# Optimization experiments

Measured on AMD Instinct MI355X. Metric: run time of the kernel, lower is better.

## Reference

```python
import jax, jax.numpy as jnp
import numpy as np

MARGIN = 1.0
EPS = 1e-6
DIAG_BIG = 99999.0


def setup_inputs() -> dict:
    key = jax.random.key(0)
    x = jax.random.normal(key, (16384, 256), dtype=jnp.float32)
    # HardNet descriptors are unit-L2 normalized (the distance formula assumes it)
    x = x / jnp.linalg.norm(x, axis=1, keepdims=True)
    return {"x": x}


def reference(x) -> jnp.ndarray:
    cnt = x.shape[0] // 2
    a = x[:cnt]          # [N, d] anchors
    p = x[cnt:]          # [N, d] positives
    # pairwise unit-L2 distance: sqrt((1 - a.p^T + eps) * 2)
    dmat = jnp.sqrt((1.0 - jnp.matmul(a, p.T) + EPS) * 2.0)  # [N, N]
    pos = jnp.diagonal(dmat)                                  # [N]
    # mask diagonal with large constant, then row/col mins = hard negatives
    masked = dmat + jnp.eye(cnt, dtype=dmat.dtype) * DIAG_BIG
    min_a = jnp.min(masked, axis=0)   # best negative anchor per positive
    min_p = jnp.min(masked, axis=1)   # best negative positive per anchor
    neg = jnp.minimum(min_a, min_p)   # [N]
    return jnp.mean(jnp.clip(MARGIN - neg + pos, 0.0))
```

## Files before the change

kernel.cpp:

```cpp
#include <hip/hip_runtime.h>
#include <hip/hip_fp8.h>


#define CNT    8192
#define KDIM   256
#define BIGF   3.0e38f
#define SCALE1 0x7F7F7F7F

typedef float f32x4  __attribute__((ext_vector_type(4)));
typedef float f32x16 __attribute__((ext_vector_type(16)));
typedef int   v8i    __attribute__((ext_vector_type(8)));

union frag8 { uint4 q[2]; v8i v; };

__device__ __forceinline__ unsigned short f2bf(float f) {
    unsigned u = __float_as_uint(f);
    u += 0x7FFFu + ((u >> 16) & 1u);
    return (unsigned short)(u >> 16);
}

__device__ __forceinline__ unsigned cvt4_fp8(float a, float b, float c, float d) {
#if __has_builtin(__builtin_amdgcn_cvt_pk_fp8_f32)
    unsigned v = __builtin_amdgcn_cvt_pk_fp8_f32(a, b, 0, false);
    v = __builtin_amdgcn_cvt_pk_fp8_f32(c, d, v, true);
    return v;
#else
    return (unsigned)__hip_fp8_e4m3(a).__x |
           ((unsigned)__hip_fp8_e4m3(b).__x << 8) |
           ((unsigned)__hip_fp8_e4m3(c).__x << 16) |
           ((unsigned)__hip_fp8_e4m3(d).__x << 24);
#endif
}


__global__ __launch_bounds__(256) void convert_mx_kernel(
    const float* __restrict__ x, unsigned char* __restrict__ xb,
    unsigned* __restrict__ mins)
{
    int T    = blockIdx.x * 256 + threadIdx.x;
    int lane = T & 63;
    int h    = (T >> 6) & 1;
    int c    = T >> 7;
    int kc64 = c & 3;
    int rg   = c >> 2;
    int row  = rg * 32 + (lane & 31);
    int col0 = kc64 * 64 + (lane >> 5) * 32 + h * 16;
    const float* src = x + (size_t)row * KDIM + col0;
    float4 u0 = *(const float4*)(src);
    float4 u1 = *(const float4*)(src + 4);
    float4 u2 = *(const float4*)(src + 8);
    float4 u3 = *(const float4*)(src + 12);
    uint4 w;
    w.x = cvt4_fp8(u0.x, u0.y, u0.z, u0.w);
    w.y = cvt4_fp8(u1.x, u1.y, u1.z, u1.w);
    w.z = cvt4_fp8(u2.x, u2.y, u2.z, u2.w);
    w.w = cvt4_fp8(u3.x, u3.y, u3.z, u3.w);
    *(uint4*)(xb + (size_t)T * 16) = w;
    if (T < 2 * CNT) mins[T] = 0x7F7FFFFFu;
}

__device__ __forceinline__ void stage_P(
    const char* __restrict__ Pb, char* lbuf, int bn, int wave, int lane)
{
    #pragma unroll
    for (int t = 0; t < 16; t++) {
        const int o   = wave * 16 + t;
        const int cc  = o >> 1;
        const int h   = o & 1;
        const int rg  = cc & 7;
        const int kcs = cc >> 3;
        const char* src = Pb + (((size_t)(bn * 8 + rg)) << 13)
                             + kcs * 2048 + h * 1024 + lane * 16;
        __builtin_amdgcn_global_load_lds(
            (const __attribute__((address_space(1))) void*)src,
            (__attribute__((address_space(3))) void*)(lbuf + cc * 2048 + h * 1024),
            16, 0, 0);
    }
}

#define TST  136
__global__ __launch_bounds__(256, 2) void dist12_kernel(
    const unsigned char* __restrict__ Ab_, const unsigned char* __restrict__ Pb_,
    unsigned* __restrict__ g_rowmin, unsigned* __restrict__ g_colmin,
    float* __restrict__ g_pos)
{
    __shared__ char smem[65536];

    const char* Ab = (const char*)Ab_;
    const char* Pb = (const char*)Pb_;

    const int tid  = threadIdx.x;
    const int l    = blockIdx.x;
    const int xcd  = l & 7;
    const int i    = l >> 3;
    const int bm   = (xcd >> 1) * 16 + (i & 15);
    const int bn   = (xcd & 1) * 16 + (i >> 4);

    const int wave = tid >> 6;
    const int lane = tid & 63;
    const int l31  = lane & 31;
    const int kh   = lane >> 5;
    const int wm   = wave >> 1;
    const int wn   = wave & 1;

    stage_P(Pb, smem, bn, wave, lane);
    __syncthreads();

    f32x16 acc[2][4];
    #pragma unroll
    for (int a = 0; a < 2; a++)
        #pragma unroll
        for (int b = 0; b < 4; b++)
            #pragma unroll
            for (int r = 0; r < 16; r++)
                acc[a][b][r] = 0.f;

    const char* Abase = Ab + lane * 16;
    size_t a_off[2];
    #pragma unroll
    for (int mi = 0; mi < 2; mi++)
        a_off[mi] = (size_t)(bm * 4 + wm * 2 + mi) << 13;

    frag8 ca[2], na[2];
    #pragma unroll
    for (int mi = 0; mi < 2; mi++) {
        ca[mi].q[0] = *(const uint4*)(Abase + a_off[mi]);
        ca[mi].q[1] = *(const uint4*)(Abase + a_off[mi] + 1024);
    }
    #pragma unroll
    for (int kc = 0; kc < 4; kc++) {
        if (kc < 3) {
            #pragma unroll
            for (int mi = 0; mi < 2; mi++) {
                na[mi].q[0] = *(const uint4*)(Abase + a_off[mi] + (kc + 1) * 2048);
                na[mi].q[1] = *(const uint4*)(Abase + a_off[mi] + (kc + 1) * 2048 + 1024);
            }
        }
        frag8 fb[4];
        #pragma unroll
        for (int ni = 0; ni < 4; ni++) {
            const char* p = smem + (kc * 8 + wn * 4 + ni) * 2048 + lane * 16;
            fb[ni].q[0] = *(const uint4*)(p);
            fb[ni].q[1] = *(const uint4*)(p + 1024);
        }
        #pragma unroll
        for (int mi = 0; mi < 2; mi++)
            #pragma unroll
            for (int ni = 0; ni < 4; ni++)
                acc[mi][ni] = __builtin_amdgcn_mfma_scale_f32_32x32x64_f8f6f4(
                    ca[mi].v, fb[ni].v, acc[mi][ni],
                    0, 0,
                    0, SCALE1,
                    0, SCALE1);
        if (kc < 3) {
            #pragma unroll
            for (int mi = 0; mi < 2; mi++) ca[mi] = na[mi];
        }
    }


    if ((bm >> 1) == bn) {
        const int dstart = (bm & 1) * 128;
        #pragma unroll
        for (int mi = 0; mi < 2; mi++)
            #pragma unroll
            for (int ni = 0; ni < 4; ni++)
                #pragma unroll
                for (int reg = 0; reg < 16; reg++) {
                    int rl = wm * 64 + mi * 32 + (reg & 3) + 8 * (reg >> 2) + 4 * kh;
                    int cl = wn * 128 + ni * 32 + l31;
                    if (cl == rl + dstart) {
                        g_pos[bm * 128 + rl] = (1.0f - acc[mi][ni][reg] + 1e-6f) * 2.0f;
                        acc[mi][ni][reg] = -BIGF;
                    }
                }
    }

    #pragma unroll
    for (int ni = 0; ni < 4; ni++) {
        float v = -BIGF;
        #pragma unroll
        for (int mi = 0; mi < 2; mi++)
            #pragma unroll
            for (int reg = 0; reg < 16; reg++)
                v = fmaxf(v, acc[mi][ni][reg]);
        v = fmaxf(v, __shfl_xor(v, 32, 64));
        if (kh == 0) {
            float tt = fmaxf((1.0f - v + 1e-6f) * 2.0f, 0.0f);
            atomicMin(&g_colmin[bn * 256 + wn * 128 + ni * 32 + l31],
                      __float_as_uint(tt));
        }
    }

    __syncthreads();
    float* T = (float*)smem;
    const int entry = wn * 32 + l31;
    #pragma unroll
    for (int mi = 0; mi < 2; mi++)
        #pragma unroll
        for (int q = 0; q < 4; q++) {
            f32x4 v;
            #pragma unroll
            for (int rr = 0; rr < 4; rr++) {
                float m = acc[mi][0][q * 4 + rr];
                #pragma unroll
                for (int ni = 1; ni < 4; ni++)
                    m = fmaxf(m, acc[mi][ni][q * 4 + rr]);
                v[rr] = m;
            }
            *(f32x4*)&T[entry * TST + wm * 64 + mi * 32 + q * 8 + kh * 4] = v;
        }
    __syncthreads();

    if (tid < 128) {
        int row = tid;
        float v0 = T[row], v1 = T[TST + row];
        #pragma unroll
        for (int e = 2; e < 64; e += 2) {
            v0 = fmaxf(v0, T[e * TST + row]);
            v1 = fmaxf(v1, T[(e + 1) * TST + row]);
        }
        float v = fmaxf(v0, v1);
        float tt = fmaxf((1.0f - v + 1e-6f) * 2.0f, 0.0f);
        atomicMin(&g_rowmin[bm * 128 + row], __float_as_uint(tt));
    }
}

__global__ __launch_bounds__(1024) void finalize_t_kernel(
    const unsigned* __restrict__ rm, const unsigned* __restrict__ cm,
    const float* __restrict__ post, float* __restrict__ out)
{
    float local = 0.f;
    for (int i = threadIdx.x; i < CNT; i += 1024) {
        float t   = fminf(__uint_as_float(rm[i]), __uint_as_float(cm[i]));
        float neg = sqrtf(fmaxf(t, 0.f));
        float pos = sqrtf(fmaxf(post[i], 0.f));
        local += fmaxf(1.0f - neg + pos, 0.0f);
    }
    #pragma unroll
    for (int m = 1; m < 64; m <<= 1) local += __shfl_xor(local, m, 64);
    __shared__ float wsum[16];
    if ((threadIdx.x & 63) == 0) wsum[threadIdx.x >> 6] = local;
    __syncthreads();
    if (threadIdx.x == 0) {
        float s = 0.f;
        #pragma unroll
        for (int w = 0; w < 16; w++) s += wsum[w];
        out[0] = s * (1.0f / (float)CNT);
    }
}


#define BM 128
#define BN 128
#define BK 64
#define KST (BK + 8)

typedef __bf16 bf16x8 __attribute__((ext_vector_type(8)));

__global__ __launch_bounds__(256) void init_min_kernel(unsigned* buf, int n) {
    int i = blockIdx.x * 256 + threadIdx.x;
    if (i < n) buf[i] = 0x7F7FFFFFu;
}

__global__ __launch_bounds__(256) void dist_tile_kernel(
    const float* __restrict__ A, const float* __restrict__ P,
    unsigned* __restrict__ g_rowmin, unsigned* __restrict__ g_colmin,
    float* __restrict__ g_pos)
{
    __shared__ unsigned short As[BM * KST];
    __shared__ unsigned short Bs[BN * KST];
    __shared__ unsigned redrow[BM];
    __shared__ unsigned redcol[BN];

    const int tid  = threadIdx.x;
    const int bm   = blockIdx.y;
    const int bn   = blockIdx.x;
    const int wave = tid >> 6;
    const int lane = tid & 63;
    const int quad = lane >> 4;
    const int l15  = lane & 15;
    const int m_off = (wave >> 1) * 64;
    const int n_off = (wave & 1) * 64;

    if (tid < BM) redrow[tid] = 0x7F7FFFFFu;
    if (tid < BN) redcol[tid] = 0x7F7FFFFFu;

    f32x4 acc[4][4];
    #pragma unroll
    for (int i = 0; i < 4; i++)
        #pragma unroll
        for (int j = 0; j < 4; j++)
            acc[i][j] = (f32x4){0.f, 0.f, 0.f, 0.f};

    const int srow = tid >> 4;
    const int scol = tid & 15;

    for (int kc = 0; kc < KDIM / BK; kc++) {
        #pragma unroll
        for (int i = 0; i < 8; i++) {
            int r = srow + i * 16;
            float4 va = *(const float4*)(A + (size_t)(bm * BM + r) * KDIM + kc * BK + scol * 4);
            float4 vb = *(const float4*)(P + (size_t)(bn * BN + r) * KDIM + kc * BK + scol * 4);
            ushort4 wa, wb;
            wa.x = f2bf(va.x); wa.y = f2bf(va.y); wa.z = f2bf(va.z); wa.w = f2bf(va.w);
            wb.x = f2bf(vb.x); wb.y = f2bf(vb.y); wb.z = f2bf(vb.z); wb.w = f2bf(vb.w);
            *(ushort4*)(&As[r * KST + scol * 4]) = wa;
            *(ushort4*)(&Bs[r * KST + scol * 4]) = wb;
        }
        __syncthreads();
        #pragma unroll
        for (int ks = 0; ks < BK / 32; ks++) {
            bf16x8 af[4], bfr[4];
            #pragma unroll
            for (int mi = 0; mi < 4; mi++)
                af[mi] = *(const bf16x8*)(&As[(m_off + mi * 16 + l15) * KST + ks * 32 + quad * 8]);
            #pragma unroll
            for (int ni = 0; ni < 4; ni++)
                bfr[ni] = *(const bf16x8*)(&Bs[(n_off + ni * 16 + l15) * KST + ks * 32 + quad * 8]);
            #pragma unroll
            for (int mi = 0; mi < 4; mi++)
                #pragma unroll
                for (int ni = 0; ni < 4; ni++)
                    acc[mi][ni] = __builtin_amdgcn_mfma_f32_16x16x32_bf16(
                        af[mi], bfr[ni], acc[mi][ni], 0, 0, 0);
        }
        __syncthreads();
    }

    float rmin[4][4], cmin[4];
    #pragma unroll
    for (int mi = 0; mi < 4; mi++)
        #pragma unroll
        for (int r = 0; r < 4; r++) rmin[mi][r] = BIGF;
    #pragma unroll
    for (int ni = 0; ni < 4; ni++) cmin[ni] = BIGF;

    const int grow0 = bm * BM + m_off + quad * 4;
    const int gcol0 = bn * BN + n_off + l15;

    #pragma unroll
    for (int mi = 0; mi < 4; mi++)
        #pragma unroll
        for (int ni = 0; ni < 4; ni++) {
            int gcol = gcol0 + ni * 16;
            #pragma unroll
            for (int r = 0; r < 4; r++) {
                int grow = grow0 + mi * 16 + r;
                float s = acc[mi][ni][r];
                float d = sqrtf((1.0f - s + 1e-6f) * 2.0f);
                float dm = d;
                if (grow == gcol) { g_pos[grow] = d; dm = BIGF; }
                rmin[mi][r] = fminf(rmin[mi][r], dm);
                cmin[ni]    = fminf(cmin[ni], dm);
            }
        }

    #pragma unroll
    for (int mi = 0; mi < 4; mi++)
        #pragma unroll
        for (int r = 0; r < 4; r++) {
            float v = rmin[mi][r];
            v = fminf(v, __shfl_xor(v, 1, 64));
            v = fminf(v, __shfl_xor(v, 2, 64));
            v = fminf(v, __shfl_xor(v, 4, 64));
            v = fminf(v, __shfl_xor(v, 8, 64));
            rmin[mi][r] = v;
        }
    #pragma unroll
    for (int ni = 0; ni < 4; ni++) {
        float v = cmin[ni];
        v = fminf(v, __shfl_xor(v, 16, 64));
        v = fminf(v, __shfl_xor(v, 32, 64));
        cmin[ni] = v;
    }

    if (l15 == 0) {
        #pragma unroll
        for (int mi = 0; mi < 4; mi++)
            #pragma unroll
            for (int r = 0; r < 4; r++)
                atomicMin(&redrow[m_off + mi * 16 + quad * 4 + r],
                          __float_as_uint(rmin[mi][r]));
    }
    if (quad == 0) {
        #pragma unroll
        for (int ni = 0; ni < 4; ni++)
            atomicMin(&redcol[n_off + ni * 16 + l15], __float_as_uint(cmin[ni]));
    }
    __syncthreads();

    if (tid < 128) atomicMin(&g_rowmin[bm * BM + tid], redrow[tid]);
    else           atomicMin(&g_colmin[bn * BN + (tid - 128)], redcol[tid - 128]);
}

__global__ __launch_bounds__(1024) void finalize_kernel(
    const unsigned* __restrict__ g_rowmin, const unsigned* __restrict__ g_colmin,
    const float* __restrict__ g_pos, float* __restrict__ out)
{
    float local = 0.f;
    for (int i = threadIdx.x; i < CNT; i += 1024) {
        float neg = fminf(__uint_as_float(g_rowmin[i]), __uint_as_float(g_colmin[i]));
        float v = 1.0f - neg + g_pos[i];
        local += fmaxf(v, 0.0f);
    }
    #pragma unroll
    for (int m = 1; m < 64; m <<= 1) local += __shfl_xor(local, m, 64);
    __shared__ float wsum[16];
    if ((threadIdx.x & 63) == 0) wsum[threadIdx.x >> 6] = local;
    __syncthreads();
    if (threadIdx.x == 0) {
        float s = 0.f;
        #pragma unroll
        for (int w = 0; w < 16; w++) s += wsum[w];
        out[0] = s * (1.0f / (float)CNT);
    }
}


extern "C" void kernel_launch(void* const* d_in, const int* in_sizes, int n_in,
                              void* d_out, int out_size, void* d_ws, size_t ws_size,
                              hipStream_t stream) {
    const float* x = (const float*)d_in[0];
    float* out = (float*)d_out;

    const size_t fp8_bytes = (size_t)2 * CNT * KDIM;
    const size_t need = fp8_bytes + (size_t)2 * CNT * 4 + (size_t)CNT * 4;

    if (ws_size >= need) {
        unsigned char* xb   = (unsigned char*)d_ws;
        unsigned*      mins = (unsigned*)((char*)d_ws + fp8_bytes);
        float*         pos  = (float*)(mins + 2 * CNT);
        convert_mx_kernel<<<dim3(1024), dim3(256), 0, stream>>>(x, xb, mins);
        dist12_kernel<<<dim3(2048), dim3(256), 0, stream>>>(
            xb, xb + (size_t)CNT * KDIM, mins, mins + CNT, pos);
        finalize_t_kernel<<<dim3(1), dim3(1024), 0, stream>>>(mins, mins + CNT, pos, out);
    } else {
        unsigned* rowmin = (unsigned*)d_ws;
        unsigned* colmin = rowmin + CNT;
        float*    pos    = (float*)(colmin + CNT);
        init_min_kernel<<<dim3(2 * CNT / 256), dim3(256), 0, stream>>>(rowmin, 2 * CNT);
        dist_tile_kernel<<<dim3(CNT / BN, CNT / BM), dim3(256), 0, stream>>>(
            x, x + (size_t)CNT * KDIM, rowmin, colmin, pos);
        finalize_kernel<<<dim3(1), dim3(1024), 0, stream>>>(rowmin, colmin, pos, out);
    }
}
```

Baseline: 92.29 us.

## Loop each block over four A tiles reusing staged P tile in LDS

Each block now stages its 256-column P tile into LDS once and iterates over four 128-row A tiles, cutting the grid from 2048 to 512 blocks and reusing the staged P data. The row-min reduction switches from a transposed LDS table with two barriers to shuffle reduction plus LDS atomicMin into a per-block buffer, flushed to global once at the end. This reduces P staging traffic and global row atomics, but lowers block count and parallelism, may leave CUs underfilled, and serializes the tiles within a block.

```diff
diff --git a/kernel.cpp b/kernel.cpp
--- a/kernel.cpp
+++ b/kernel.cpp
@@ -78,13 +78,14 @@
     }
 }
 
-#define TST  136
-__global__ __launch_bounds__(256, 2) void dist12_kernel(
+#define NTILE 4
+__global__ __launch_bounds__(256, 2) void dist14_kernel(
     const unsigned char* __restrict__ Ab_, const unsigned char* __restrict__ Pb_,
     unsigned* __restrict__ g_rowmin, unsigned* __restrict__ g_colmin,
     float* __restrict__ g_pos)
 {
     __shared__ char smem[65536];
+    __shared__ unsigned redrow[NTILE * 128];
 
     const char* Ab = (const char*)Ab_;
     const char* Pb = (const char*)Pb_;
@@ -93,8 +94,8 @@
     const int l    = blockIdx.x;
     const int xcd  = l & 7;
     const int i    = l >> 3;
-    const int bm   = (xcd >> 1) * 16 + (i & 15);
-    const int bn   = (xcd & 1) * 16 + (i >> 4);
+    const int bn   = i & 31;
+    const int bmg  = xcd * 2 + (i >> 5);
 
     const int wave = tid >> 6;
     const int lane = tid & 63;
@@ -104,125 +105,128 @@
     const int wn   = wave & 1;
 
     stage_P(Pb, smem, bn, wave, lane);
+    redrow[tid]       = 0x7F7FFFFFu;
+    redrow[tid + 256] = 0x7F7FFFFFu;
     __syncthreads();
 
-    f32x16 acc[2][4];
-    #pragma unroll
-    for (int a = 0; a < 2; a++)
-        #pragma unroll
-        for (int b = 0; b < 4; b++)
-            #pragma unroll
-            for (int r = 0; r < 16; r++)
-                acc[a][b][r] = 0.f;
-
     const char* Abase = Ab + lane * 16;
-    size_t a_off[2];
-    #pragma unroll
-    for (int mi = 0; mi < 2; mi++)
-        a_off[mi] = (size_t)(bm * 4 + wm * 2 + mi) << 13;
-
-    frag8 ca[2], na[2];
-    #pragma unroll
-    for (int mi = 0; mi < 2; mi++) {
-        ca[mi].q[0] = *(const uint4*)(Abase + a_off[mi]);
-        ca[mi].q[1] = *(const uint4*)(Abase + a_off[mi] + 1024);
-    }
-    #pragma unroll
-    for (int kc = 0; kc < 4; kc++) {
-        if (kc < 3) {
-            #pragma unroll
-            for (int mi = 0; mi < 2; mi++) {
-                na[mi].q[0] = *(const uint4*)(Abase + a_off[mi] + (kc + 1) * 2048);
-                na[mi].q[1] = *(const uint4*)(Abase + a_off[mi] + (kc + 1) * 2048 + 1024);
-            }
-        }
-        frag8 fb[4];
+
+    #pragma unroll 1
+    for (int g = 0; g < NTILE; g++) {
+        const int bm = bmg * NTILE + g;
+
+        f32x16 acc[2][4];
+        #pragma unroll
+        for (int a = 0; a < 2; a++)
+            #pragma unroll
+            for (int b = 0; b < 4; b++)
+                #pragma unroll
+                for (int r = 0; r < 16; r++)
+                    acc[a][b][r] = 0.f;
+
+        size_t a_off[2];
+        #pragma unroll
+        for (int mi = 0; mi < 2; mi++)
+            a_off[mi] = (size_t)(bm * 4 + wm * 2 + mi) << 13;
+
+        frag8 ca[2], na[2];
+        #pragma unroll
+        for (int mi = 0; mi < 2; mi++) {
+            ca[mi].q[0] = *(const uint4*)(Abase + a_off[mi]);
+            ca[mi].q[1] = *(const uint4*)(Abase + a_off[mi] + 1024);
+        }
+        #pragma unroll
+        for (int kc = 0; kc < 4; kc++) {
+            if (kc < 3) {
+                #pragma unroll
+                for (int mi = 0; mi < 2; mi++) {
+                    na[mi].q[0] = *(const uint4*)(Abase + a_off[mi] + (kc + 1) * 2048);
+                    na[mi].q[1] = *(const uint4*)(Abase + a_off[mi] + (kc + 1) * 2048 + 1024);
+                }
+            }
+            frag8 fb[4];
+            #pragma unroll
+            for (int ni = 0; ni < 4; ni++) {
+                const char* p = smem + (kc * 8 + wn * 4 + ni) * 2048 + lane * 16;
+                fb[ni].q[0] = *(const uint4*)(p);
+                fb[ni].q[1] = *(const uint4*)(p + 1024);
+            }
+            #pragma unroll
+            for (int mi = 0; mi < 2; mi++)
+                #pragma unroll
+                for (int ni = 0; ni < 4; ni++)
+                    acc[mi][ni] = __builtin_amdgcn_mfma_scale_f32_32x32x64_f8f6f4(
+                        ca[mi].v, fb[ni].v, acc[mi][ni],
+                        0, 0,
+                        0, SCALE1,
+                        0, SCALE1);
+            if (kc < 3) {
+                #pragma unroll
+                for (int mi = 0; mi < 2; mi++) ca[mi] = na[mi];
+            }
+        }
+
+
+        if ((bm >> 1) == bn) {
+            const int dstart = (bm & 1) * 128;
+            #pragma unroll
+            for (int mi = 0; mi < 2; mi++)
+                #pragma unroll
+                for (int ni = 0; ni < 4; ni++)
+                    #pragma unroll
+                    for (int reg = 0; reg < 16; reg++) {
+                        int rl = wm * 64 + mi * 32 + (reg & 3) + 8 * (reg >> 2) + 4 * kh;
+                        int cl = wn * 128 + ni * 32 + l31;
+                        if (cl == rl + dstart) {
+                            g_pos[bm * 128 + rl] = (1.0f - acc[mi][ni][reg] + 1e-6f) * 2.0f;
+                            acc[mi][ni][reg] = -BIGF;
+                        }
+                    }
+        }
+
         #pragma unroll
         for (int ni = 0; ni < 4; ni++) {
-            const char* p = smem + (kc * 8 + wn * 4 + ni) * 2048 + lane * 16;
-            fb[ni].q[0] = *(const uint4*)(p);
-            fb[ni].q[1] = *(const uint4*)(p + 1024);
-        }
+            float v = -BIGF;
+            #pragma unroll
+            for (int mi = 0; mi < 2; mi++)
+                #pragma unroll
+                for (int reg = 0; reg < 16; reg++)
+                    v = fmaxf(v, acc[mi][ni][reg]);
+            v = fmaxf(v, __shfl_xor(v, 32, 64));
+            if (kh == 0) {
+                float tt = fmaxf((1.0f - v + 1e-6f) * 2.0f, 0.0f);
+                atomicMin(&g_colmin[bn * 256 + wn * 128 + ni * 32 + l31],
+                          __float_as_uint(tt));
+            }
+        }
+
         #pragma unroll
         for (int mi = 0; mi < 2; mi++)
             #pragma unroll
-            for (int ni = 0; ni < 4; ni++)
-                acc[mi][ni] = __builtin_amdgcn_mfma_scale_f32_32x32x64_f8f6f4(
-                    ca[mi].v, fb[ni].v, acc[mi][ni],
-                    0, 0,
-                    0, SCALE1,
-                    0, SCALE1);
-        if (kc < 3) {
-            #pragma unroll
-            for (int mi = 0; mi < 2; mi++) ca[mi] = na[mi];
-        }
-    }
-
-
-    if ((bm >> 1) == bn) {
-        const int dstart = (bm & 1) * 128;
-        #pragma unroll
-        for (int mi = 0; mi < 2; mi++)
-            #pragma unroll
-            for (int ni = 0; ni < 4; ni++)
-                #pragma unroll
-                for (int reg = 0; reg < 16; reg++) {
+            for (int reg = 0; reg < 16; reg++) {
+                float v = acc[mi][0][reg];
+                #pragma unroll
+                for (int ni = 1; ni < 4; ni++)
+                    v = fmaxf(v, acc[mi][ni][reg]);
+                v = fmaxf(v, __shfl_xor(v, 1, 64));
+                v = fmaxf(v, __shfl_xor(v, 2, 64));
+                if ((l31 & 3) == 0) {
                     int rl = wm * 64 + mi * 32 + (reg & 3) + 8 * (reg >> 2) + 4 * kh;
-                    int cl = wn * 128 + ni * 32 + l31;
-                    if (cl == rl + dstart) {
-                        g_pos[bm * 128 + rl] = (1.0f - acc[mi][ni][reg] + 1e-6f) * 2.0f;
-                        acc[mi][ni][reg] = -BIGF;
-                    }
+                    float tt = fmaxf((1.0f - v + 1e-6f) * 2.0f, 0.0f);
+                    atomicMin(&redrow[g * 128 + rl], __float_as_uint(tt));
                 }
-    }
-
-    #pragma unroll
-    for (int ni = 0; ni < 4; ni++) {
-        float v = -BIGF;
-        #pragma unroll
-        for (int mi = 0; mi < 2; mi++)
-            #pragma unroll
-            for (int reg = 0; reg < 16; reg++)
-                v = fmaxf(v, acc[mi][ni][reg]);
-        v = fmaxf(v, __shfl_xor(v, 32, 64));
-        if (kh == 0) {
-            float tt = fmaxf((1.0f - v + 1e-6f) * 2.0f, 0.0f);
-            atomicMin(&g_colmin[bn * 256 + wn * 128 + ni * 32 + l31],
-                      __float_as_uint(tt));
-        }
+            }
     }
 
     __syncthreads();
-    float* T = (float*)smem;
-    const int entry = wn * 32 + l31;
-    #pragma unroll
-    for (int mi = 0; mi < 2; mi++)
-        #pragma unroll
-        for (int q = 0; q < 4; q++) {
-            f32x4 v;
-            #pragma unroll
-            for (int rr = 0; rr < 4; rr++) {
-                float m = acc[mi][0][q * 4 + rr];
-                #pragma unroll
-                for (int ni = 1; ni < 4; ni++)
-                    m = fmaxf(m, acc[mi][ni][q * 4 + rr]);
-                v[rr] = m;
-            }
-            *(f32x4*)&T[entry * TST + wm * 64 + mi * 32 + q * 8 + kh * 4] = v;
-        }
-    __syncthreads();
-
-    if (tid < 128) {
-        int row = tid;
-        float v0 = T[row], v1 = T[TST + row];
-        #pragma unroll
-        for (int e = 2; e < 64; e += 2) {
-            v0 = fmaxf(v0, T[e * TST + row]);
-            v1 = fmaxf(v1, T[(e + 1) * TST + row]);
-        }
-        float v = fmaxf(v0, v1);
-        float tt = fmaxf((1.0f - v + 1e-6f) * 2.0f, 0.0f);
-        atomicMin(&g_rowmin[bm * 128 + row], __float_as_uint(tt));
+    {
+        int idx = tid;
+        #pragma unroll
+        for (int r = 0; r < 2; r++, idx += 256) {
+            int g  = idx >> 7;
+            int rl = idx & 127;
+            atomicMin(&g_rowmin[(bmg * NTILE + g) * 128 + rl], redrow[idx]);
+        }
     }
 }
 
@@ -432,7 +436,7 @@
         unsigned*      mins = (unsigned*)((char*)d_ws + fp8_bytes);
         float*         pos  = (float*)(mins + 2 * CNT);
         convert_mx_kernel<<<dim3(1024), dim3(256), 0, stream>>>(x, xb, mins);
-        dist12_kernel<<<dim3(2048), dim3(256), 0, stream>>>(
+        dist14_kernel<<<dim3(512), dim3(256), 0, stream>>>(
             xb, xb + (size_t)CNT * KDIM, mins, mins + CNT, pos);
         finalize_t_kernel<<<dim3(1), dim3(1024), 0, stream>>>(mins, mins + CNT, pos, out);
     } else {
```

After: 122.9 us. 1.33x slower.

## Replace atomicMin reductions with per-tile partial buffers and two-stage finalize

Applied to the files above, without the earlier changes.

The distance kernel no longer issues global atomicMin for row and column minima. Each tile writes its partial minima to dedicated slots in workspace buffers (32 row partials and 64 column partials per index). A 32-block finalize pass reduces them, and a tiny second kernel sums the block results, replacing the single-block finalize. This removes atomic contention and the min-buffer initialization, at the cost of about 3 MB of extra partial-buffer traffic and one more kernel launch.

```diff
diff --git a/kernel.cpp b/kernel.cpp
--- a/kernel.cpp
+++ b/kernel.cpp
@@ -34,8 +34,7 @@
 
 
 __global__ __launch_bounds__(256) void convert_mx_kernel(
-    const float* __restrict__ x, unsigned char* __restrict__ xb,
-    unsigned* __restrict__ mins)
+    const float* __restrict__ x, unsigned char* __restrict__ xb)
 {
     int T    = blockIdx.x * 256 + threadIdx.x;
     int lane = T & 63;
@@ -56,7 +55,6 @@
     w.z = cvt4_fp8(u2.x, u2.y, u2.z, u2.w);
     w.w = cvt4_fp8(u3.x, u3.y, u3.z, u3.w);
     *(uint4*)(xb + (size_t)T * 16) = w;
-    if (T < 2 * CNT) mins[T] = 0x7F7FFFFFu;
 }
 
 __device__ __forceinline__ void stage_P(
@@ -79,9 +77,9 @@
 }
 
 #define TST  136
-__global__ __launch_bounds__(256, 2) void dist12_kernel(
+__global__ __launch_bounds__(256, 2) void dist15_kernel(
     const unsigned char* __restrict__ Ab_, const unsigned char* __restrict__ Pb_,
-    unsigned* __restrict__ g_rowmin, unsigned* __restrict__ g_colmin,
+    float* __restrict__ rowpart, float* __restrict__ colpart,
     float* __restrict__ g_pos)
 {
     __shared__ char smem[65536];
@@ -187,8 +185,7 @@
         v = fmaxf(v, __shfl_xor(v, 32, 64));
         if (kh == 0) {
             float tt = fmaxf((1.0f - v + 1e-6f) * 2.0f, 0.0f);
-            atomicMin(&g_colmin[bn * 256 + wn * 128 + ni * 32 + l31],
-                      __float_as_uint(tt));
+            colpart[bm * (2 * CNT / 2) + bn * 256 + wn * 128 + ni * 32 + l31] = tt;
         }
     }
 
@@ -222,32 +219,42 @@
         }
         float v = fmaxf(v0, v1);
         float tt = fmaxf((1.0f - v + 1e-6f) * 2.0f, 0.0f);
-        atomicMin(&g_rowmin[bm * 128 + row], __float_as_uint(tt));
-    }
-}
-
-__global__ __launch_bounds__(1024) void finalize_t_kernel(
-    const unsigned* __restrict__ rm, const unsigned* __restrict__ cm,
-    const float* __restrict__ post, float* __restrict__ out)
-{
-    float local = 0.f;
-    for (int i = threadIdx.x; i < CNT; i += 1024) {
-        float t   = fminf(__uint_as_float(rm[i]), __uint_as_float(cm[i]));
-        float neg = sqrtf(fmaxf(t, 0.f));
-        float pos = sqrtf(fmaxf(post[i], 0.f));
-        local += fmaxf(1.0f - neg + pos, 0.0f);
-    }
+        rowpart[bn * CNT + bm * 128 + row] = tt;
+    }
+}
+
+__global__ __launch_bounds__(256) void finalize1_kernel(
+    const float* __restrict__ rowpart, const float* __restrict__ colpart,
+    const float* __restrict__ post, float* __restrict__ psum)
+{
+    const int i = blockIdx.x * 256 + threadIdx.x;
+    float rv = BIGF, cv = BIGF;
+    #pragma unroll
+    for (int bn = 0; bn < 32; bn++)
+        rv = fminf(rv, rowpart[bn * CNT + i]);
+    #pragma unroll
+    for (int bm = 0; bm < 64; bm++)
+        cv = fminf(cv, colpart[bm * CNT + i]);
+    float t   = fminf(rv, cv);
+    float neg = sqrtf(fmaxf(t, 0.f));
+    float pos = sqrtf(fmaxf(post[i], 0.f));
+    float local = fmaxf(1.0f - neg + pos, 0.0f);
     #pragma unroll
     for (int m = 1; m < 64; m <<= 1) local += __shfl_xor(local, m, 64);
-    __shared__ float wsum[16];
+    __shared__ float wsum[4];
     if ((threadIdx.x & 63) == 0) wsum[threadIdx.x >> 6] = local;
     __syncthreads();
-    if (threadIdx.x == 0) {
-        float s = 0.f;
-        #pragma unroll
-        for (int w = 0; w < 16; w++) s += wsum[w];
-        out[0] = s * (1.0f / (float)CNT);
-    }
+    if (threadIdx.x == 0)
+        psum[blockIdx.x] = wsum[0] + wsum[1] + wsum[2] + wsum[3];
+}
+
+__global__ __launch_bounds__(64) void finalize2_kernel(
+    const float* __restrict__ psum, float* __restrict__ out)
+{
+    float local = (threadIdx.x < 32) ? psum[threadIdx.x] : 0.f;
+    #pragma unroll
+    for (int m = 1; m < 64; m <<= 1) local += __shfl_xor(local, m, 64);
+    if (threadIdx.x == 0) out[0] = local * (1.0f / (float)CNT);
 }
 
 
@@ -425,16 +432,21 @@
     float* out = (float*)d_out;
 
     const size_t fp8_bytes = (size_t)2 * CNT * KDIM;
-    const size_t need = fp8_bytes + (size_t)2 * CNT * 4 + (size_t)CNT * 4;
+    const size_t part_f    = (size_t)(32 + 64) * CNT;
+    const size_t need = fp8_bytes + part_f * 4 + (size_t)CNT * 4 + 32 * 4;
 
     if (ws_size >= need) {
-        unsigned char* xb   = (unsigned char*)d_ws;
-        unsigned*      mins = (unsigned*)((char*)d_ws + fp8_bytes);
-        float*         pos  = (float*)(mins + 2 * CNT);
-        convert_mx_kernel<<<dim3(1024), dim3(256), 0, stream>>>(x, xb, mins);
-        dist12_kernel<<<dim3(2048), dim3(256), 0, stream>>>(
-            xb, xb + (size_t)CNT * KDIM, mins, mins + CNT, pos);
-        finalize_t_kernel<<<dim3(1), dim3(1024), 0, stream>>>(mins, mins + CNT, pos, out);
+        unsigned char* xb      = (unsigned char*)d_ws;
+        float*         rowpart = (float*)((char*)d_ws + fp8_bytes);
+        float*         colpart = rowpart + (size_t)32 * CNT;
+        float*         pos     = colpart + (size_t)64 * CNT;
+        float*         psum    = pos + CNT;
+        convert_mx_kernel<<<dim3(1024), dim3(256), 0, stream>>>(x, xb);
+        dist15_kernel<<<dim3(2048), dim3(256), 0, stream>>>(
+            xb, xb + (size_t)CNT * KDIM, rowpart, colpart, pos);
+        finalize1_kernel<<<dim3(32), dim3(256), 0, stream>>>(
+            rowpart, colpart, pos, psum);
+        finalize2_kernel<<<dim3(1), dim3(64), 0, stream>>>(psum, out);
     } else {
         unsigned* rowmin = (unsigned*)d_ws;
         unsigned* colmin = rowmin + CNT;
```

Result: no change. 91.80 us (-0.5%).
